# Optimization experiments

Hardware: AMD Instinct MI355X
Metric: run time of the kernel (lower is better)

## Reference

```python
import jax, jax.numpy as jnp
import numpy as np

T, B, E, H = 2048, 2, 1024, 16
HD = E // H
NEG = -1e9  # large negative for causal additive mask


def setup_inputs() -> dict:
    key = jax.random.key(0)
    ks = jax.random.split(key, 6)
    s = 0.02
    query = jax.random.normal(ks[0], (T, B, E), jnp.float32)
    # causal additive mask, as commonly passed to this module's attn_mask arg
    attn_mask = jnp.triu(jnp.full((T, T), NEG, jnp.float32), k=1)
    key_padding_mask = jnp.zeros((B, T), jnp.bool_)
    Wq = jax.random.normal(ks[1], (E, E), jnp.float32) * s
    Wk = jax.random.normal(ks[2], (E, E), jnp.float32) * s
    Wv = jax.random.normal(ks[3], (E, E), jnp.float32) * s
    Wo = jax.random.normal(ks[4], (E, E), jnp.float32) * s
    bq = jnp.zeros((E,), jnp.float32)
    bk = jnp.zeros((E,), jnp.float32)
    bv = jnp.zeros((E,), jnp.float32)
    bo = jnp.zeros((E,), jnp.float32)
    return {"query": query, "attn_mask": attn_mask, "key_padding_mask": key_padding_mask,
            "Wq": Wq, "bq": bq, "Wk": Wk, "bk": bk, "Wv": Wv, "bv": bv, "Wo": Wo, "bo": bo}


def _shape(x):
    # [T, B, E] -> [B*H, T, HD]; E splits as (H, HD), flat index = b*H + h
    return x.reshape(T, B * H, HD).transpose(1, 0, 2)


def reference(query, attn_mask, key_padding_mask, Wq, bq, Wk, bk, Wv, bv, Wo, bo):
    scaling = HD ** -0.5
    q = (query @ Wq.T + bq) * scaling  # scale q as in torch code
    k = query @ Wk.T + bk              # self-attention path (static_kv=False)
    v = query @ Wv.T + bv
    q, k, v = _shape(q), _shape(k), _shape(v)            # [B*H, T, HD]
    w = jnp.einsum('bth,bsh->bts', q, k)                  # [B*H, T, S]
    w = w.reshape(B, H, T, T) + attn_mask                 # additive mask broadcast
    w = jnp.where(key_padding_mask[:, None, None, :], -jnp.inf, w)
    p = jax.nn.softmax(w, axis=-1).reshape(B * H, T, T)   # dropout p=0 (eval)
    o = jnp.einsum('bts,bsh->bth', p, v)                  # [B*H, T, HD]
    o = o.transpose(1, 0, 2).reshape(T, B, E)
    return o @ Wo.T + bo
```

## Files before the change

### kernel.cpp

```cpp
#include <hip/hip_runtime.h>

#define Tt 2048
#define Bb 2
#define Ee 1024
#define Hh 16
#define HD 64
#define BH 32

typedef __attribute__((ext_vector_type(8))) short short8;
typedef __attribute__((ext_vector_type(4))) short short4v;
typedef __attribute__((ext_vector_type(8))) __bf16 bf16x8;
typedef __attribute__((ext_vector_type(4))) float floatx4;

#define OFF_X  0
#define OFF_WQ 4194304
#define OFF_WK 5242880
#define OFF_WV 6291456
#define OFF_WO 7340032
#define OFF_Q  8388608
#define OFF_K  12582912
#define OFF_V  16777216
#define OFF_O  20971520

__device__ __forceinline__ short f2bf(float f) {
  union { float f; unsigned u; } a; a.f = f;
  unsigned r = a.u + 0x7fffu + ((a.u >> 16) & 1u);
  return (short)(r >> 16);
}

__device__ __forceinline__ floatx4 mfma16(short8 a, short8 b, floatx4 c) {
  return __builtin_amdgcn_mfma_f32_16x16x32_bf16(
      __builtin_bit_cast(bf16x8, a), __builtin_bit_cast(bf16x8, b), c, 0, 0, 0);
}

__device__ __forceinline__ floatx4 mfma_k16(short4v a, short4v b, floatx4 c) {
#if __has_builtin(__builtin_amdgcn_mfma_f32_16x16x16bf16_1k)
  return __builtin_amdgcn_mfma_f32_16x16x16bf16_1k(a, b, c, 0, 0, 0);
#else
  floatx4 d;
  asm("v_mfma_f32_16x16x16_bf16 %0, %1, %2, %3" : "=v"(d) : "v"(a), "v"(b), "v"(c));
  return d;
#endif
}

__device__ __forceinline__ void gl_lds16(const short* g, short* l) {
  __builtin_amdgcn_global_load_lds(
      (const __attribute__((address_space(1))) void*)g,
      (__attribute__((address_space(3))) void*)l, 16, 0, 0);
}

__device__ __forceinline__ uint2 exppack(floatx4 s, float& l) {
  float p0 = __builtin_amdgcn_exp2f(s[0]);
  float p1 = __builtin_amdgcn_exp2f(s[1]);
  float p2 = __builtin_amdgcn_exp2f(s[2]);
  float p3 = __builtin_amdgcn_exp2f(s[3]);
  l += (p0 + p1) + (p2 + p3);
  unsigned u0 = __builtin_bit_cast(unsigned, p0) + 0x8000u;
  unsigned u1 = __builtin_bit_cast(unsigned, p1) + 0x8000u;
  unsigned u2 = __builtin_bit_cast(unsigned, p2) + 0x8000u;
  unsigned u3 = __builtin_bit_cast(unsigned, p3) + 0x8000u;
  uint2 pk;
  pk.x = __builtin_amdgcn_perm(u1, u0, 0x07060302u);
  pk.y = __builtin_amdgcn_perm(u3, u2, 0x07060302u);
  return pk;
}

__global__ __launch_bounds__(256)
void convert_kernel(const float* __restrict__ x, const float* __restrict__ wq,
                    const float* __restrict__ wk, const float* __restrict__ wv,
                    const float* __restrict__ wo, short* __restrict__ dst)
{
  const int i4 = blockIdx.x * 256 + threadIdx.x;
  const int f = i4 * 4;
  const float* src;
  int local;
  if (f < 4194304) { src = x; local = f; }
  else {
    int gg = f - 4194304;
    int wsel = gg >> 20;
    local = gg & 1048575;
    src = (wsel == 0) ? wq : (wsel == 1) ? wk : (wsel == 2) ? wv : wo;
  }
  floatx4 v = *reinterpret_cast<const floatx4*>(src + local);
  short4 o;
  o.x = f2bf(v[0]); o.y = f2bf(v[1]); o.z = f2bf(v[2]); o.w = f2bf(v[3]);
  *reinterpret_cast<short4*>(dst + f) = o;
}

__global__ __launch_bounds__(256, 2)
void qkv_kernel(short* __restrict__ ws, const float* __restrict__ bq,
                const float* __restrict__ bk, const float* __restrict__ bv)
{
  __shared__ short smem[2][8192];
  const int t = threadIdx.x;
  const int lane = t & 63;
  const int w = t >> 6;
  const int g = lane >> 4, c = lane & 15;
  const int rb = blockIdx.x * 128;
  const int cb = blockIdx.y * 128;
  const int rw = (w >> 1) * 64, cw2 = (w & 1) * 64;

  const short* gA[2]; const short* gB[2]; int oC[2];
#pragma unroll
  for (int i = 0; i < 2; i++) {
    const int cid = t + 256 * i;
    const int row = cid >> 2;
    const int lch = (cid & 3) ^ ((row + (row >> 2)) & 3);
    gA[i] = ws + OFF_X + (rb + row) * 1024 + lch * 8;
    gB[i] = ws + OFF_WQ + (cb + row) * 1024 + lch * 8;
    oC[i] = cid * 8;
  }
  const int xr = (g ^ ((c + (c >> 2)) & 3)) * 8;

  floatx4 acc[4][4];
#pragma unroll
  for (int i = 0; i < 4; i++)
#pragma unroll
    for (int j = 0; j < 4; j++) acc[i][j] = (floatx4){0.f, 0.f, 0.f, 0.f};

#pragma unroll
  for (int i = 0; i < 2; i++) {
    gl_lds16(gA[i], &smem[0][oC[i]]);
    gl_lds16(gB[i], &smem[0][4096 + oC[i]]);
  }
  __syncthreads();

  for (int kt = 0; kt < 32; kt++) {
    const int cur = kt & 1;
    if (kt < 31) {
      const int kn = (kt + 1) * 32;
#pragma unroll
      for (int i = 0; i < 2; i++) {
        gl_lds16(gA[i] + kn, &smem[cur ^ 1][oC[i]]);
        gl_lds16(gB[i] + kn, &smem[cur ^ 1][4096 + oC[i]]);
      }
    }
    short8 af[4], bf[4];
#pragma unroll
    for (int mi = 0; mi < 4; mi++)
      af[mi] = *reinterpret_cast<const short8*>(&smem[cur][(rw + mi * 16 + c) * 32 + xr]);
#pragma unroll
    for (int ni = 0; ni < 4; ni++)
      bf[ni] = *reinterpret_cast<const short8*>(&smem[cur][4096 + (cw2 + ni * 16 + c) * 32 + xr]);
#pragma unroll
    for (int mi = 0; mi < 4; mi++)
#pragma unroll
      for (int ni = 0; ni < 4; ni++)
        acc[mi][ni] = mfma16(af[mi], bf[ni], acc[mi][ni]);
    __syncthreads();
  }

  const int m = cb >> 10;
  const int lcb = cb & 1023;
  if (m < 2) {
#pragma unroll
    for (int ni = 0; ni < 4; ni++) {
      const int lc = lcb + cw2 + ni * 16 + c;
      const int h = lc >> 6, d = lc & 63;
      const float bcol = (m == 0 ? bq : bk)[lc];
#pragma unroll
      for (int mi = 0; mi < 4; mi++)
#pragma unroll
        for (int r = 0; r < 4; r++) {
          const int row = rb + rw + mi * 16 + g * 4 + r;
          const int tt = row >> 1, b = row & 1;
          float v = acc[mi][ni][r] + bcol;
          if (m == 0) v *= 0.18033688f;
          ws[(m == 0 ? OFF_Q : OFF_K) + ((b * Hh + h) * Tt + tt) * HD + d] = f2bf(v);
        }
    }
  } else {
    short* vt = &smem[0][0];
    const int hb = lcb >> 6;
    for (int b = 0; b < 2; b++) {
      __syncthreads();
#pragma unroll
      for (int ni = 0; ni < 4; ni++) {
        const int lcol = cw2 + ni * 16 + c;
        const float bcol = bv[lcb + lcol];
#pragma unroll
        for (int mi = 0; mi < 4; mi++)
#pragma unroll
          for (int rr = 0; rr < 2; rr++) {
            const int r = rr * 2 + b;
            const int rloc = rw + mi * 16 + g * 4 + r;
            vt[lcol * 72 + (rloc >> 1)] = f2bf(acc[mi][ni][r] + bcol);
          }
      }
      __syncthreads();
#pragma unroll
      for (int i = 0; i < 4; i++) {
        const int u = t + 256 * i;
        const int lcol = u >> 3, seg = u & 7;
        short8 vv = *reinterpret_cast<const short8*>(vt + lcol * 72 + seg * 8);
        const int h = hb + (lcol >> 6), d = lcol & 63;
        *reinterpret_cast<short8*>(ws + OFF_V + ((b * Hh + h) * HD + d) * Tt
                                   + (rb >> 1) + seg * 8) = vv;
      }
    }
  }
}

__global__ __launch_bounds__(256, 2)
void gemm_o(const short* __restrict__ ws, const float* __restrict__ bo,
            float* __restrict__ dout)
{
  __shared__ short smem[2][8192];
  const int t = threadIdx.x;
  const int lane = t & 63;
  const int w = t >> 6;
  const int g = lane >> 4, c = lane & 15;
  const int rb = blockIdx.x * 128;
  const int cb = blockIdx.y * 128;
  const int rw = (w >> 1) * 64, cw2 = (w & 1) * 64;

  const short* gA[2]; const short* gB[2]; int oC[2];
#pragma unroll
  for (int i = 0; i < 2; i++) {
    const int cid = t + 256 * i;
    const int row = cid >> 2;
    const int lch = (cid & 3) ^ ((row + (row >> 2)) & 3);
    gA[i] = ws + OFF_O + (rb + row) * 1024 + lch * 8;
    gB[i] = ws + OFF_WO + (cb + row) * 1024 + lch * 8;
    oC[i] = cid * 8;
  }
  const int xr = (g ^ ((c + (c >> 2)) & 3)) * 8;

  floatx4 acc[4][4];
#pragma unroll
  for (int i = 0; i < 4; i++)
#pragma unroll
    for (int j = 0; j < 4; j++) acc[i][j] = (floatx4){0.f, 0.f, 0.f, 0.f};

#pragma unroll
  for (int i = 0; i < 2; i++) {
    gl_lds16(gA[i], &smem[0][oC[i]]);
    gl_lds16(gB[i], &smem[0][4096 + oC[i]]);
  }
  __syncthreads();

  for (int kt = 0; kt < 32; kt++) {
    const int cur = kt & 1;
    if (kt < 31) {
      const int kn = (kt + 1) * 32;
#pragma unroll
      for (int i = 0; i < 2; i++) {
        gl_lds16(gA[i] + kn, &smem[cur ^ 1][oC[i]]);
        gl_lds16(gB[i] + kn, &smem[cur ^ 1][4096 + oC[i]]);
      }
    }
    short8 af[4], bf[4];
#pragma unroll
    for (int mi = 0; mi < 4; mi++)
      af[mi] = *reinterpret_cast<const short8*>(&smem[cur][(rw + mi * 16 + c) * 32 + xr]);
#pragma unroll
    for (int ni = 0; ni < 4; ni++)
      bf[ni] = *reinterpret_cast<const short8*>(&smem[cur][4096 + (cw2 + ni * 16 + c) * 32 + xr]);
#pragma unroll
    for (int mi = 0; mi < 4; mi++)
#pragma unroll
      for (int ni = 0; ni < 4; ni++)
        acc[mi][ni] = mfma16(af[mi], bf[ni], acc[mi][ni]);
    __syncthreads();
  }

#pragma unroll
  for (int ni = 0; ni < 4; ni++) {
    const int col = cb + cw2 + ni * 16 + c;
    const float bcol = bo[col];
#pragma unroll
    for (int mi = 0; mi < 4; mi++)
#pragma unroll
      for (int r = 0; r < 4; r++) {
        const int row = rb + rw + mi * 16 + g * 4 + r;
        dout[row * 1024 + col] = acc[mi][ni][r] + bcol;
      }
  }
}

__global__ __launch_bounds__(256, 2)
void attn_kernel(short* __restrict__ ws, const unsigned char* __restrict__ kpm)
{
  __shared__ __align__(16) char smem[35840];
  float* bufA = reinterpret_cast<float*>(smem);
  float* bufB = reinterpret_cast<float*>(smem + 17408);
  float* Ls   = reinterpret_cast<float*>(smem + 34816);

  const int t = threadIdx.x;
  const int lane = t & 63;
  const int w = t >> 6;
  const int g = lane >> 4, c = lane & 15;
  const int bh = blockIdx.x;
  const int b = bh >> 4;
  const int h = bh & 15;
  const int qt = 31 - (int)blockIdx.y;
  const int qrow0 = qt * 64;

  const short* Qp = ws + OFF_Q + bh * Tt * HD;
  const short* Kp = ws + OFF_K + bh * Tt * HD;
  const short* Vp = ws + OFF_V + bh * HD * Tt;

  short8 qf[4][2];
#pragma unroll
  for (int qs = 0; qs < 4; qs++) {
    const short* qr = Qp + (qrow0 + qs * 16 + c) * HD + g * 8;
    qf[qs][0] = *reinterpret_cast<const short8*>(qr);
    qf[qs][1] = *reinterpret_cast<const short8*>(qr + 32);
  }

  const uint4* kpv = reinterpret_cast<const uint4*>(kpm + b * Tt);
  uint4 k0v = kpv[lane * 2], k1v = kpv[lane * 2 + 1];
  const bool nz = (k0v.x | k0v.y | k0v.z | k0v.w | k1v.x | k1v.y | k1v.z | k1v.w) != 0;
  const unsigned long long kpany = __ballot(nz);

  float lt[4] = {0.f, 0.f, 0.f, 0.f};
  floatx4 acc[4][4];
#pragma unroll
  for (int i = 0; i < 4; i++)
#pragma unroll
    for (int j = 0; j < 4; j++) acc[i][j] = (floatx4){0.f, 0.f, 0.f, 0.f};

  const short* Kw = Kp + (w * 16 + c) * HD + g * 8;
  const short* Vl = Vp + c * Tt + w * 16 + g * 4;

  const int NT = qt + 1, NP = NT >> 1, TAIL = NT & 1;

  for (int pt = 0; pt < NP; pt++) {
    const int ta = 2 * pt, tb = ta + 1;
    const short* kap = Kw + ta * 4096;
    const short* kbp = Kw + tb * 4096;
    short8 kA0 = *reinterpret_cast<const short8*>(kap);
    short8 kA1 = *reinterpret_cast<const short8*>(kap + 32);
    short8 kB0 = *reinterpret_cast<const short8*>(kbp);
    short8 kB1 = *reinterpret_cast<const short8*>(kbp + 32);
    short4v vA[4], vB[4];
#pragma unroll
    for (int dt = 0; dt < 4; dt++) {
      vA[dt] = *reinterpret_cast<const short4v*>(Vl + dt * 16 * Tt + ta * 64);
      vB[dt] = *reinterpret_cast<const short4v*>(Vl + dt * 16 * Tt + tb * 64);
    }
    floatx4 sa[4], sb[4];
#pragma unroll
    for (int qs = 0; qs < 4; qs++) {
      floatx4 z = (floatx4){0.f, 0.f, 0.f, 0.f};
      z = mfma16(kA0, qf[qs][0], z);
      z = mfma16(kA1, qf[qs][1], z);
      sa[qs] = z;
    }
#pragma unroll
    for (int qs = 0; qs < 4; qs++) {
      floatx4 z = (floatx4){0.f, 0.f, 0.f, 0.f};
      z = mfma16(kB0, qf[qs][0], z);
      z = mfma16(kB1, qf[qs][1], z);
      sb[qs] = z;
    }
    if ((kpany >> (2 * ta)) & 3ULL) {
#pragma unroll
      for (int r = 0; r < 4; r++)
        if (kpm[b * Tt + ta * 64 + w * 16 + g * 4 + r] != 0) {
#pragma unroll
          for (int qs = 0; qs < 4; qs++) sa[qs][r] = -1e30f;
        }
    }
    if ((kpany >> (2 * tb)) & 3ULL) {
#pragma unroll
      for (int r = 0; r < 4; r++)
        if (kpm[b * Tt + tb * 64 + w * 16 + g * 4 + r] != 0) {
#pragma unroll
          for (int qs = 0; qs < 4; qs++) sb[qs][r] = -1e30f;
        }
    }
    if (tb == qt) {
      const int kl = w * 16 + g * 4;
#pragma unroll
      for (int qs = 0; qs < 4; qs++)
#pragma unroll
        for (int r = 0; r < 4; r++)
          if (kl + r > qs * 16 + c) sb[qs][r] = -1e30f;
    }
    short8 pa8[4];
#pragma unroll
    for (int qs = 0; qs < 4; qs++) {
      uint2 ua = exppack(sa[qs], lt[qs]);
      uint2 ub = exppack(sb[qs], lt[qs]);
      uint4 uu; uu.x = ua.x; uu.y = ua.y; uu.z = ub.x; uu.w = ub.y;
      pa8[qs] = __builtin_bit_cast(short8, uu);
    }
    short8 vb8[4];
#pragma unroll
    for (int dt = 0; dt < 4; dt++) {
      short8 vv;
      vv[0] = vA[dt][0]; vv[1] = vA[dt][1]; vv[2] = vA[dt][2]; vv[3] = vA[dt][3];
      vv[4] = vB[dt][0]; vv[5] = vB[dt][1]; vv[6] = vB[dt][2]; vv[7] = vB[dt][3];
      vb8[dt] = vv;
    }
#pragma unroll
    for (int qs = 0; qs < 4; qs++)
#pragma unroll
      for (int dt = 0; dt < 4; dt++)
        acc[qs][dt] = mfma16(pa8[qs], vb8[dt], acc[qs][dt]);
  }

  if (TAIL) {
    const int ta = NT - 1;
    const short* kap = Kw + ta * 4096;
    short8 kA0 = *reinterpret_cast<const short8*>(kap);
    short8 kA1 = *reinterpret_cast<const short8*>(kap + 32);
    short4v vA[4];
#pragma unroll
    for (int dt = 0; dt < 4; dt++)
      vA[dt] = *reinterpret_cast<const short4v*>(Vl + dt * 16 * Tt + ta * 64);
    floatx4 st[4];
#pragma unroll
    for (int qs = 0; qs < 4; qs++) {
      floatx4 z = (floatx4){0.f, 0.f, 0.f, 0.f};
      z = mfma16(kA0, qf[qs][0], z);
      z = mfma16(kA1, qf[qs][1], z);
      st[qs] = z;
    }
    if ((kpany >> (2 * ta)) & 3ULL) {
#pragma unroll
      for (int r = 0; r < 4; r++)
        if (kpm[b * Tt + ta * 64 + w * 16 + g * 4 + r] != 0) {
#pragma unroll
          for (int qs = 0; qs < 4; qs++) st[qs][r] = -1e30f;
        }
    }
    {
      const int kl = w * 16 + g * 4;
#pragma unroll
      for (int qs = 0; qs < 4; qs++)
#pragma unroll
        for (int r = 0; r < 4; r++)
          if (kl + r > qs * 16 + c) st[qs][r] = -1e30f;
    }
    short4v pa4[4];
#pragma unroll
    for (int qs = 0; qs < 4; qs++) {
      uint2 u = exppack(st[qs], lt[qs]);
      pa4[qs] = __builtin_bit_cast(short4v, u);
    }
#pragma unroll
    for (int qs = 0; qs < 4; qs++)
#pragma unroll
      for (int dt = 0; dt < 4; dt++)
        acc[qs][dt] = mfma_k16(pa4[qs], vA[dt], acc[qs][dt]);
  }

#pragma unroll
  for (int qs = 0; qs < 4; qs++) {
    lt[qs] += __shfl_xor(lt[qs], 16);
    lt[qs] += __shfl_xor(lt[qs], 32);
  }
  if (g == 0) {
#pragma unroll
    for (int qs = 0; qs < 4; qs++) Ls[w * 64 + qs * 16 + c] = lt[qs];
  }
  float* mybuf = (w < 2) ? bufA : bufB;
  if ((w & 1) == 0) {
#pragma unroll
    for (int qs = 0; qs < 4; qs++)
#pragma unroll
      for (int dt = 0; dt < 4; dt++)
#pragma unroll
        for (int r = 0; r < 4; r++)
          mybuf[(qs * 16 + g * 4 + r) * 68 + dt * 16 + c] = acc[qs][dt][r];
  }
  __syncthreads();
  if (w & 1) {
#pragma unroll
    for (int qs = 0; qs < 4; qs++)
#pragma unroll
      for (int dt = 0; dt < 4; dt++)
#pragma unroll
        for (int r = 0; r < 4; r++)
          mybuf[(qs * 16 + g * 4 + r) * 68 + dt * 16 + c] += acc[qs][dt][r];
  }
  __syncthreads();
  const int row = w * 16 + (lane >> 2);
  const int dseg = (lane & 3) * 16;
  const float inv = 1.f / (Ls[row] + Ls[64 + row] + Ls[128 + row] + Ls[192 + row]);
  short* op = ws + OFF_O + ((qrow0 + row) * Bb + b) * Ee + h * 64 + dseg;
#pragma unroll
  for (int i = 0; i < 2; i++) {
    floatx4 a0 = *reinterpret_cast<const floatx4*>(&bufA[row * 68 + dseg + i * 8]);
    floatx4 a1 = *reinterpret_cast<const floatx4*>(&bufA[row * 68 + dseg + i * 8 + 4]);
    floatx4 b0 = *reinterpret_cast<const floatx4*>(&bufB[row * 68 + dseg + i * 8]);
    floatx4 b1 = *reinterpret_cast<const floatx4*>(&bufB[row * 68 + dseg + i * 8 + 4]);
    short8 s;
#pragma unroll
    for (int j = 0; j < 4; j++) s[j] = f2bf((a0[j] + b0[j]) * inv);
#pragma unroll
    for (int j = 0; j < 4; j++) s[4 + j] = f2bf((a1[j] + b1[j]) * inv);
    *reinterpret_cast<short8*>(op + i * 8) = s;
  }
}

extern "C" void kernel_launch(void* const* d_in, const int* in_sizes, int n_in,
                              void* d_out, int out_size, void* d_ws, size_t ws_size,
                              hipStream_t stream)
{
  const float* query = (const float*)d_in[0];
  const unsigned char* kpm = (const unsigned char*)d_in[2];
  const float* Wq = (const float*)d_in[3];
  const float* bq = (const float*)d_in[4];
  const float* Wk = (const float*)d_in[5];
  const float* bk = (const float*)d_in[6];
  const float* Wv = (const float*)d_in[7];
  const float* bv = (const float*)d_in[8];
  const float* Wo = (const float*)d_in[9];
  const float* bo = (const float*)d_in[10];
  short* ws = (short*)d_ws;
  float* out = (float*)d_out;

  convert_kernel<<<dim3(8192), dim3(256), 0, stream>>>(query, Wq, Wk, Wv, Wo, ws);
  qkv_kernel<<<dim3(32, 24), dim3(256), 0, stream>>>(ws, bq, bk, bv);
  attn_kernel<<<dim3(32, 32), dim3(256), 0, stream>>>(ws, kpm);
  gemm_o<<<dim3(32, 8), dim3(256), 0, stream>>>(ws, bo, out);
}
```

Before: 206.0 us.

## Store Q/K/V in MFMA-fragment tiled layout and prefetch K tiles in attention

The projection kernel now writes Q, K and V into a blocked layout of 16-row by 64-dim tiles, so each lane's MFMA fragment is one contiguous 16-byte chunk and a wavefront reads contiguous memory. The attention kernel loads K for the next tile pair one iteration ahead, splits the score computation so only one score buffer is live at a time, and raises launch bounds to 3 blocks per CU. The aim is to cut uncoalesced global loads and hide load latency with more occupancy. The risks are register spills under the tighter register budget, and that any other reader of these buffers must agree on the new layout.

```diff
diff --git a/kernel.cpp b/kernel.cpp
--- a/kernel.cpp
+++ b/kernel.cpp
@@ -158,6 +158,7 @@
       const int lc = lcb + cw2 + ni * 16 + c;
       const int h = lc >> 6, d = lc & 63;
       const float bcol = (m == 0 ? bq : bk)[lc];
+      const int dpart = (d >> 3) * 128 + (d & 7);
 #pragma unroll
       for (int mi = 0; mi < 4; mi++)
 #pragma unroll
@@ -166,7 +167,8 @@
           const int tt = row >> 1, b = row & 1;
           float v = acc[mi][ni][r] + bcol;
           if (m == 0) v *= 0.18033688f;
-          ws[(m == 0 ? OFF_Q : OFF_K) + ((b * Hh + h) * Tt + tt) * HD + d] = f2bf(v);
+          ws[(m == 0 ? OFF_Q : OFF_K) + (b * Hh + h) * 131072
+             + (tt >> 4) * 1024 + dpart + (tt & 15) * 8] = f2bf(v);
         }
     }
   } else {
@@ -194,8 +196,9 @@
         const int lcol = u >> 3, seg = u & 7;
         short8 vv = *reinterpret_cast<const short8*>(vt + lcol * 72 + seg * 8);
         const int h = hb + (lcol >> 6), d = lcol & 63;
-        *reinterpret_cast<short8*>(ws + OFF_V + ((b * Hh + h) * HD + d) * Tt
-                                   + (rb >> 1) + seg * 8) = vv;
+        *reinterpret_cast<short8*>(ws + OFF_V + ((b * Hh + h)) * 131072
+                                   + ((rb >> 5) + (seg >> 1)) * 1024
+                                   + d * 16 + (seg & 1) * 8) = vv;
       }
     }
   }
@@ -278,7 +281,7 @@
   }
 }
 
-__global__ __launch_bounds__(256, 2)
+__global__ __launch_bounds__(256, 3)
 void attn_kernel(short* __restrict__ ws, const unsigned char* __restrict__ kpm)
 {
   __shared__ __align__(16) char smem[35840];
@@ -296,16 +299,16 @@
   const int qt = 31 - (int)blockIdx.y;
   const int qrow0 = qt * 64;
 
-  const short* Qp = ws + OFF_Q + bh * Tt * HD;
-  const short* Kp = ws + OFF_K + bh * Tt * HD;
-  const short* Vp = ws + OFF_V + bh * HD * Tt;
+  const short* Qp = ws + OFF_Q + bh * 131072;
+  const short* Kp = ws + OFF_K + bh * 131072;
+  const short* Vp = ws + OFF_V + bh * 131072;
 
   short8 qf[4][2];
+  const short* Qc = Qp + (qrow0 >> 4) * 1024 + lane * 8;
 #pragma unroll
   for (int qs = 0; qs < 4; qs++) {
-    const short* qr = Qp + (qrow0 + qs * 16 + c) * HD + g * 8;
-    qf[qs][0] = *reinterpret_cast<const short8*>(qr);
-    qf[qs][1] = *reinterpret_cast<const short8*>(qr + 32);
+    qf[qs][0] = *reinterpret_cast<const short8*>(Qc + qs * 1024);
+    qf[qs][1] = *reinterpret_cast<const short8*>(Qc + qs * 1024 + 512);
   }
 
   const uint4* kpv = reinterpret_cast<const uint4*>(kpm + b * Tt);
@@ -320,54 +323,72 @@
 #pragma unroll
     for (int j = 0; j < 4; j++) acc[i][j] = (floatx4){0.f, 0.f, 0.f, 0.f};
 
-  const short* Kw = Kp + (w * 16 + c) * HD + g * 8;
-  const short* Vl = Vp + c * Tt + w * 16 + g * 4;
+  const short* Kl = Kp + w * 1024 + lane * 8;
+  const short* Vl = Vp + w * 1024 + c * 16 + g * 4;
 
   const int NT = qt + 1, NP = NT >> 1, TAIL = NT & 1;
+
+  short8 kc0, kc1, kc2, kc3;
+  kc0 = *reinterpret_cast<const short8*>(Kl);
+  kc1 = *reinterpret_cast<const short8*>(Kl + 512);
+  if (NP > 0) {
+    kc2 = *reinterpret_cast<const short8*>(Kl + 4096);
+    kc3 = *reinterpret_cast<const short8*>(Kl + 4096 + 512);
+  } else { kc2 = kc0; kc3 = kc1; }
+  short8 kn0 = kc0, kn1 = kc1, kn2 = kc2, kn3 = kc3;
 
   for (int pt = 0; pt < NP; pt++) {
     const int ta = 2 * pt, tb = ta + 1;
-    const short* kap = Kw + ta * 4096;
-    const short* kbp = Kw + tb * 4096;
-    short8 kA0 = *reinterpret_cast<const short8*>(kap);
-    short8 kA1 = *reinterpret_cast<const short8*>(kap + 32);
-    short8 kB0 = *reinterpret_cast<const short8*>(kbp);
-    short8 kB1 = *reinterpret_cast<const short8*>(kbp + 32);
+    const short* va = Vl + ta * 4096;
     short4v vA[4], vB[4];
 #pragma unroll
     for (int dt = 0; dt < 4; dt++) {
-      vA[dt] = *reinterpret_cast<const short4v*>(Vl + dt * 16 * Tt + ta * 64);
-      vB[dt] = *reinterpret_cast<const short4v*>(Vl + dt * 16 * Tt + tb * 64);
-    }
-    floatx4 sa[4], sb[4];
+      vA[dt] = *reinterpret_cast<const short4v*>(va + dt * 256);
+      vB[dt] = *reinterpret_cast<const short4v*>(va + 4096 + dt * 256);
+    }
+    if (pt + 1 < NP) {
+      const short* kp_ = Kl + (ta + 2) * 4096;
+      kn0 = *reinterpret_cast<const short8*>(kp_);
+      kn1 = *reinterpret_cast<const short8*>(kp_ + 512);
+      kn2 = *reinterpret_cast<const short8*>(kp_ + 4096);
+      kn3 = *reinterpret_cast<const short8*>(kp_ + 4096 + 512);
+    } else if (TAIL) {
+      const short* kp_ = Kl + (ta + 2) * 4096;
+      kn0 = *reinterpret_cast<const short8*>(kp_);
+      kn1 = *reinterpret_cast<const short8*>(kp_ + 512);
+    }
+    floatx4 s[4];
 #pragma unroll
     for (int qs = 0; qs < 4; qs++) {
       floatx4 z = (floatx4){0.f, 0.f, 0.f, 0.f};
-      z = mfma16(kA0, qf[qs][0], z);
-      z = mfma16(kA1, qf[qs][1], z);
-      sa[qs] = z;
-    }
+      z = mfma16(kc0, qf[qs][0], z);
+      z = mfma16(kc1, qf[qs][1], z);
+      s[qs] = z;
+    }
+    if ((kpany >> (2 * ta)) & 3ULL) {
+#pragma unroll
+      for (int r = 0; r < 4; r++)
+        if (kpm[b * Tt + ta * 64 + w * 16 + g * 4 + r] != 0) {
+#pragma unroll
+          for (int qs = 0; qs < 4; qs++) s[qs][r] = -1e30f;
+        }
+    }
+    uint2 ua[4];
+#pragma unroll
+    for (int qs = 0; qs < 4; qs++) ua[qs] = exppack(s[qs], lt[qs]);
 #pragma unroll
     for (int qs = 0; qs < 4; qs++) {
       floatx4 z = (floatx4){0.f, 0.f, 0.f, 0.f};
-      z = mfma16(kB0, qf[qs][0], z);
-      z = mfma16(kB1, qf[qs][1], z);
-      sb[qs] = z;
-    }
-    if ((kpany >> (2 * ta)) & 3ULL) {
-#pragma unroll
-      for (int r = 0; r < 4; r++)
-        if (kpm[b * Tt + ta * 64 + w * 16 + g * 4 + r] != 0) {
-#pragma unroll
-          for (int qs = 0; qs < 4; qs++) sa[qs][r] = -1e30f;
-        }
+      z = mfma16(kc2, qf[qs][0], z);
+      z = mfma16(kc3, qf[qs][1], z);
+      s[qs] = z;
     }
     if ((kpany >> (2 * tb)) & 3ULL) {
 #pragma unroll
       for (int r = 0; r < 4; r++)
         if (kpm[b * Tt + tb * 64 + w * 16 + g * 4 + r] != 0) {
 #pragma unroll
-          for (int qs = 0; qs < 4; qs++) sb[qs][r] = -1e30f;
+          for (int qs = 0; qs < 4; qs++) s[qs][r] = -1e30f;
         }
     }
     if (tb == qt) {
@@ -376,46 +397,40 @@
       for (int qs = 0; qs < 4; qs++)
 #pragma unroll
         for (int r = 0; r < 4; r++)
-          if (kl + r > qs * 16 + c) sb[qs][r] = -1e30f;
+          if (kl + r > qs * 16 + c) s[qs][r] = -1e30f;
     }
     short8 pa8[4];
 #pragma unroll
     for (int qs = 0; qs < 4; qs++) {
-      uint2 ua = exppack(sa[qs], lt[qs]);
-      uint2 ub = exppack(sb[qs], lt[qs]);
-      uint4 uu; uu.x = ua.x; uu.y = ua.y; uu.z = ub.x; uu.w = ub.y;
+      uint2 ub = exppack(s[qs], lt[qs]);
+      uint4 uu; uu.x = ua[qs].x; uu.y = ua[qs].y; uu.z = ub.x; uu.w = ub.y;
       pa8[qs] = __builtin_bit_cast(short8, uu);
     }
-    short8 vb8[4];
 #pragma unroll
     for (int dt = 0; dt < 4; dt++) {
       short8 vv;
       vv[0] = vA[dt][0]; vv[1] = vA[dt][1]; vv[2] = vA[dt][2]; vv[3] = vA[dt][3];
       vv[4] = vB[dt][0]; vv[5] = vB[dt][1]; vv[6] = vB[dt][2]; vv[7] = vB[dt][3];
-      vb8[dt] = vv;
-    }
-#pragma unroll
-    for (int qs = 0; qs < 4; qs++)
-#pragma unroll
-      for (int dt = 0; dt < 4; dt++)
-        acc[qs][dt] = mfma16(pa8[qs], vb8[dt], acc[qs][dt]);
+#pragma unroll
+      for (int qs = 0; qs < 4; qs++)
+        acc[qs][dt] = mfma16(pa8[qs], vv, acc[qs][dt]);
+    }
+    kc0 = kn0; kc1 = kn1; kc2 = kn2; kc3 = kn3;
   }
 
   if (TAIL) {
     const int ta = NT - 1;
-    const short* kap = Kw + ta * 4096;
-    short8 kA0 = *reinterpret_cast<const short8*>(kap);
-    short8 kA1 = *reinterpret_cast<const short8*>(kap + 32);
+    const short* va = Vl + ta * 4096;
     short4v vA[4];
 #pragma unroll
     for (int dt = 0; dt < 4; dt++)
-      vA[dt] = *reinterpret_cast<const short4v*>(Vl + dt * 16 * Tt + ta * 64);
+      vA[dt] = *reinterpret_cast<const short4v*>(va + dt * 256);
     floatx4 st[4];
 #pragma unroll
     for (int qs = 0; qs < 4; qs++) {
       floatx4 z = (floatx4){0.f, 0.f, 0.f, 0.f};
-      z = mfma16(kA0, qf[qs][0], z);
-      z = mfma16(kA1, qf[qs][1], z);
+      z = mfma16(kc0, qf[qs][0], z);
+      z = mfma16(kc1, qf[qs][1], z);
       st[qs] = z;
     }
     if ((kpany >> (2 * ta)) & 3ULL) {
```

Result: faster. 201.2 us (-2.3%).
